# Performance work log

Hardware: AMD Instinct MI355X
Metric: run time of the kernel (lower is better)

Reference implementation:

```python
import jax, jax.numpy as jnp
import numpy as np

N, E = 50000, 800000          # nodes, edges (avg degree 16)
D_IN, D_H, D_OUT = 128, 128, 64
BN_EPS = 1e-5


def setup_inputs() -> dict:
    key = jax.random.key(0)
    ks = jax.random.split(key, 8)
    g = lambda k, shp, s: jax.random.normal(k, shp, jnp.float32) * s
    return {
        "x": jax.random.normal(ks[0], (N, D_IN), jnp.float32),
        "edge_index": jax.random.randint(ks[1], (2, E), 0, N),
        # SAGEConv layer 1: lin_l (neighbors, with bias), lin_r (root, no bias)
        "Wl1": g(ks[2], (D_IN, D_H), 0.05),
        "Wr1": g(ks[3], (D_IN, D_H), 0.05),
        "b1": jnp.zeros((D_H,), jnp.float32),
        # BatchNorm1d(hidden)
        "gamma": jnp.ones((D_H,), jnp.float32),
        "beta": jnp.zeros((D_H,), jnp.float32),
        # SAGEConv layer 2
        "Wl2": g(ks[4], (D_H, D_OUT), 0.05),
        "Wr2": g(ks[5], (D_H, D_OUT), 0.05),
        "b2": jnp.zeros((D_OUT,), jnp.float32),
    }


def _sage_conv(x, src, dst, Wl, Wr, b):
    """PyG SAGEConv (mean aggr): lin_l(mean_{j in N(i)} x_j) + lin_r(x_i)."""
    n = x.shape[0]
    agg = jax.ops.segment_sum(x[src], dst, num_segments=n)            # [N, d]
    cnt = jax.ops.segment_sum(jnp.ones((src.shape[0],), x.dtype), dst,
                              num_segments=n)                          # [N]
    agg = agg / jnp.maximum(cnt, 1.0)[:, None]                         # mean, 0 for isolated
    return agg @ Wl + x @ Wr + b


def _batch_norm(x, gamma, beta):
    """Training-mode BatchNorm1d: batch stats over the node axis, biased var."""
    mu = jnp.mean(x, axis=0)
    var = jnp.var(x, axis=0)
    return gamma * (x - mu) * jax.lax.rsqrt(var + BN_EPS) + beta


def reference(x, edge_index, Wl1, Wr1, b1, gamma, beta, Wl2, Wr2, b2):
    src, dst = edge_index[0], edge_index[1]
    h = _sage_conv(x, src, dst, Wl1, Wr1, b1)
    h = jax.nn.relu(_batch_norm(h, gamma, beta))
    # dropout is identity in eval / deterministic reference
    return _sage_conv(h, src, dst, Wl2, Wr2, b2)
```

## Files before the change

### kernel.cpp

```cpp
#include <hip/hip_runtime.h>
#include <hip/hip_bf16.h>
#include <hip/hip_fp8.h>

#define DIN   128
#define DH    128
#define DOUTC 64
#define BN_EPS 1e-5f

typedef __attribute__((ext_vector_type(8))) short bf16x8;
typedef __attribute__((ext_vector_type(4))) float f32x4;
typedef __attribute__((ext_vector_type(2))) float f32x2;

#ifndef __has_builtin
#define __has_builtin(x) 0
#endif
#if __has_builtin(__builtin_amdgcn_cvt_pk_f32_fp8) && __has_builtin(__builtin_amdgcn_cvt_pk_fp8_f32)
#define HW_FP8 1
#else
#define HW_FP8 0
#endif

__device__ inline unsigned short f2bf(float f) {
    __hip_bfloat16 b = __float2bfloat16(f);
    return *reinterpret_cast<unsigned short*>(&b);
}
__device__ inline float bf2f(unsigned short u) {
    return __uint_as_float(((unsigned int)u) << 16);
}
__device__ inline void fp8x4_to_f32(unsigned int w, float* o) {
#if HW_FP8
    f32x2 lo = __builtin_amdgcn_cvt_pk_f32_fp8((int)w, false);
    f32x2 hi = __builtin_amdgcn_cvt_pk_f32_fp8((int)w, true);
    o[0] = lo.x; o[1] = lo.y; o[2] = hi.x; o[3] = hi.y;
#else
    #pragma unroll
    for (int c = 0; c < 4; ++c) {
        __hip_fp8_e4m3 q; q.__x = (__hip_fp8_storage_t)((w >> (8 * c)) & 0xFF);
        o[c] = (float)q;
    }
#endif
}
__device__ inline unsigned int f32x4_to_fp8(float a, float b, float c, float d) {
#if HW_FP8
    int p = __builtin_amdgcn_cvt_pk_fp8_f32(a, b, 0, false);
    p = __builtin_amdgcn_cvt_pk_fp8_f32(c, d, p, true);
    return (unsigned int)p;
#else
    __hip_fp8_e4m3 qa(a), qb(b), qc(c), qd(d);
    return (unsigned int)qa.__x | ((unsigned int)qb.__x << 8) |
           ((unsigned int)qc.__x << 16) | ((unsigned int)qd.__x << 24);
#endif
}

__device__ inline void block_excl_scan_256(const int* __restrict__ arr,
                                           int* __restrict__ excl,
                                           int* __restrict__ wsum, int tid)
{
    int lane = tid & 63, w = tid >> 6;
    int v = arr[tid];
    int inc = v;
    #pragma unroll
    for (int off = 1; off < 64; off <<= 1) {
        int t = __shfl_up(inc, off, 64);
        if (lane >= off) inc += t;
    }
    if (lane == 63) wsum[w] = inc;
    __syncthreads();
    if (tid == 0) {
        int s = 0;
        #pragma unroll
        for (int i = 0; i < 4; ++i) { int t = wsum[i]; wsum[i] = s; s += t; }
    }
    __syncthreads();
    excl[tid] = inc - v + wsum[w];
    __syncthreads();
}

__global__ __launch_bounds__(256) void prep_kernel(
    const float* __restrict__ x, unsigned short* __restrict__ xb,
    unsigned char* __restrict__ xq,
    const float* __restrict__ Wl1, const float* __restrict__ Wr1,
    const float* __restrict__ Wl2, const float* __restrict__ Wr2,
    unsigned short* __restrict__ W1p, unsigned short* __restrict__ W2p,
    const int* __restrict__ ei, int* __restrict__ cursor,
    unsigned int* __restrict__ coarse,
    int total8, int cvtB, int E, int nb, int cap)
{
    __shared__ int hist[256], lstart[256], gbase[256], wsum[4];
    __shared__ unsigned int staged[4096];
    const int b = blockIdx.x;
    const int tid = threadIdx.x;

    if (b < cvtB) {
        int i = b * 256 + tid;
        if (i >= total8) return;
        float4 a = ((const float4*)x)[2 * i];
        float4 c = ((const float4*)x)[2 * i + 1];
        unsigned short t[8];
        t[0]=f2bf(a.x); t[1]=f2bf(a.y); t[2]=f2bf(a.z); t[3]=f2bf(a.w);
        t[4]=f2bf(c.x); t[5]=f2bf(c.y); t[6]=f2bf(c.z); t[7]=f2bf(c.w);
        *(uint4*)(xb + (size_t)i * 8) = *(uint4*)t;
        uint2 pk;
        pk.x = f32x4_to_fp8(a.x, a.y, a.z, a.w);
        pk.y = f32x4_to_fp8(c.x, c.y, c.z, c.w);
        *(uint2*)(xq + (size_t)i * 8) = pk;
        return;
    }
    if (b < cvtB + 192) {
        int region = (b - cvtB) >> 6;
        int idx = ((b - cvtB) & 63) * 256 + tid;
        int k = idx >> 7, c = idx & 127;
        int d = ((k >> 5) * 8 + (c >> 4)) * 512 + ((k >> 3) & 3) * 128 + (c & 15) * 8 + (k & 7);
        if (region == 0)      W1p[d] = f2bf(Wl1[idx]);
        else if (region == 1) W1p[128 * 128 + d] = f2bf(Wr1[idx]);
        else {
            float v = (c < 64) ? Wl2[k * 64 + c] : Wr2[k * 64 + (c - 64)];
            W2p[d] = f2bf(v);
        }
        return;
    }

    const int chunkBase = (b - cvtB - 192) * 4096;
    hist[tid] = 0;
    __syncthreads();

    unsigned int rec[16]; int pos[16]; int bb[16];
    #pragma unroll
    for (int i = 0; i < 16; ++i) {
        int e = chunkBase + i * 256 + tid;
        if (e < E) {
            int s = ei[e], d = ei[E + e];
            rec[i] = ((unsigned int)d << 16) | (unsigned int)s;
            bb[i]  = d >> 8;
            pos[i] = atomicAdd(&hist[bb[i]], 1);
        } else bb[i] = -1;
    }
    __syncthreads();

    block_excl_scan_256(hist, lstart, wsum, tid);

    if (tid < nb) {
        int c = hist[tid];
        gbase[tid] = c ? atomicAdd(&cursor[tid], c) : 0;
    }
    __syncthreads();

    #pragma unroll
    for (int i = 0; i < 16; ++i)
        if (bb[i] >= 0) staged[lstart[bb[i]] + pos[i]] = rec[i];
    __syncthreads();

    int total = min(4096, E - chunkBase);
    for (int i = tid; i < total; i += 256) {
        unsigned int r = staged[i];
        int bk  = (int)(r >> 24);
        int gp  = gbase[bk] + (i - lstart[bk]);
        if (gp < cap) coarse[(size_t)bk * cap + gp] = r;
    }
}

__global__ __launch_bounds__(256) void bin_fine(
    const int* __restrict__ cursor, const unsigned int* __restrict__ coarse,
    unsigned short* __restrict__ sorted, int* __restrict__ deg,
    int* __restrict__ row_start, int n, int cap)
{
    __shared__ int hist[256], pstart[256], cur2[256], wsum[4];
    const int b = blockIdx.x, tid = threadIdx.x;
    const int cnt = min(cursor[b], cap);
    const unsigned int* src = coarse + (size_t)b * cap;

    hist[tid] = 0;
    __syncthreads();

    int nIter = (cnt + 255) >> 8;
    for (int i = 0; i < nIter; ++i) {
        int idx = i * 256 + tid;
        if (idx < cnt) atomicAdd(&hist[(src[idx] >> 16) & 255], 1);
    }
    __syncthreads();

    block_excl_scan_256(hist, pstart, wsum, tid);
    cur2[tid] = pstart[tid];
    __syncthreads();

    for (int i = 0; i < nIter; ++i) {
        int idx = i * 256 + tid;
        if (idx < cnt) {
            unsigned int r = src[idx];
            int dl = (r >> 16) & 255;
            int p  = atomicAdd(&cur2[dl], 1);
            sorted[(size_t)b * cap + p] = (unsigned short)(r & 0xFFFFu);
        }
    }

    int node = b * 256 + tid;
    if (node < n) {
        deg[node]       = hist[tid];
        row_start[node] = b * cap + pstart[tid];
    }
}

__global__ __launch_bounds__(256) void gemm1_fused(
    const unsigned char* __restrict__ xq, const unsigned short* __restrict__ xb,
    const int* __restrict__ row_start, const int* __restrict__ deg,
    const unsigned short* __restrict__ sorted,
    const unsigned short* __restrict__ W1p, const float* __restrict__ bias,
    unsigned short* __restrict__ hb,
    float* __restrict__ bn_sum, float* __restrict__ bn_sumsq, int n)
{
    __shared__ unsigned short X[64][136];
    __shared__ unsigned short G[64][136];
    __shared__ float red[2][4][128];

    const int block_row = blockIdx.x * 64;
    const int tid  = threadIdx.x;
    const int wave = tid >> 6;
    const int lane = tid & 63;
    const int q    = lane >> 4;
    const int m16  = lane & 15;

    {
        int lr = wave * 16 + (lane >> 2);
        int g  = block_row + lr;
        #pragma unroll
        for (int i = 0; i < 4; ++i) {
            int c16 = (lane & 3) + 4 * i;
            uint4 v = {0u, 0u, 0u, 0u};
            if (g < n) v = ((const uint4*)(xb + (size_t)g * DIN))[c16];
            *(uint4*)&X[lr][c16 * 8] = v;
        }
    }

    {
        int sub = lane & 7, oct = lane >> 3;
        #pragma unroll
        for (int grp = 0; grp < 2; ++grp) {
            int lr = wave * 16 + grp * 8 + oct;
            int g  = block_row + lr;
            float acc[16];
            #pragma unroll
            for (int j = 0; j < 16; ++j) acc[j] = 0.f;
            int d = 0;
            if (g < n) {
                int base = row_start[g];
                d = deg[g];
                for (int t = 0; t < d; ++t) {
                    int s = (int)sorted[base + t];
                    uint4 raw = ((const uint4*)(xq + (size_t)s * DIN))[sub];
                    const unsigned int* w = (const unsigned int*)&raw;
                    #pragma unroll
                    for (int c = 0; c < 4; ++c) {
                        float o4[4];
                        fp8x4_to_f32(w[c], o4);
                        acc[c*4+0] += o4[0]; acc[c*4+1] += o4[1];
                        acc[c*4+2] += o4[2]; acc[c*4+3] += o4[3];
                    }
                }
            }
            float inv = 1.0f / fmaxf((float)d, 1.0f);
            unsigned short t16[16];
            #pragma unroll
            for (int j = 0; j < 16; ++j) t16[j] = f2bf(acc[j] * inv);
            *(uint4*)&G[lr][sub * 16]     = ((uint4*)t16)[0];
            *(uint4*)&G[lr][sub * 16 + 8] = ((uint4*)t16)[1];
        }
    }

    f32x4 acc[8];
    #pragma unroll
    for (int nt = 0; nt < 8; ++nt) acc[nt] = (f32x4){0.f, 0.f, 0.f, 0.f};

    #pragma unroll
    for (int ks = 0; ks < 4; ++ks) {
        bf16x8 ag = *(const bf16x8*)&G[wave * 16 + m16][ks * 32 + q * 8];
        const unsigned short* wp0 = W1p + (size_t)ks * 8 * 512;
        #pragma unroll
        for (int nt = 0; nt < 8; ++nt) {
            bf16x8 b = *(const bf16x8*)(wp0 + nt * 512 + lane * 8);
            acc[nt] = __builtin_amdgcn_mfma_f32_16x16x32_bf16(ag, b, acc[nt], 0, 0, 0);
        }
        bf16x8 ax = *(const bf16x8*)&X[wave * 16 + m16][ks * 32 + q * 8];
        const unsigned short* wp1 = W1p + (size_t)(4 + ks) * 8 * 512;
        #pragma unroll
        for (int nt = 0; nt < 8; ++nt) {
            bf16x8 b = *(const bf16x8*)(wp1 + nt * 512 + lane * 8);
            acc[nt] = __builtin_amdgcn_mfma_f32_16x16x32_bf16(ax, b, acc[nt], 0, 0, 0);
        }
    }

    float psum[8], psq[8];
    #pragma unroll
    for (int nt = 0; nt < 8; ++nt) {
        int col = nt * 16 + m16;
        float bv = bias[col];
        float s = 0.f, ssq = 0.f;
        #pragma unroll
        for (int reg = 0; reg < 4; ++reg) {
            int g = block_row + wave * 16 + q * 4 + reg;
            float v = acc[nt][reg] + bv;
            if (g < n) {
                hb[(size_t)g * DH + col] = f2bf(v);
                s += v; ssq += v * v;
            }
        }
        psum[nt] = s; psq[nt] = ssq;
    }
    #pragma unroll
    for (int nt = 0; nt < 8; ++nt) {
        psum[nt] += __shfl_xor(psum[nt], 16, 64);
        psum[nt] += __shfl_xor(psum[nt], 32, 64);
        psq[nt]  += __shfl_xor(psq[nt], 16, 64);
        psq[nt]  += __shfl_xor(psq[nt], 32, 64);
    }
    if (lane < 16) {
        #pragma unroll
        for (int nt = 0; nt < 8; ++nt) {
            red[0][wave][nt * 16 + lane] = psum[nt];
            red[1][wave][nt * 16 + lane] = psq[nt];
        }
    }
    __syncthreads();
    if (tid < 128) {
        float s = red[0][0][tid] + red[0][1][tid] + red[0][2][tid] + red[0][3][tid];
        float ssq = red[1][0][tid] + red[1][1][tid] + red[1][2][tid] + red[1][3][tid];
        atomicAdd(&bn_sum[tid], s);
        atomicAdd(&bn_sumsq[tid], ssq);
    }
}

__global__ __launch_bounds__(256) void gemm2p_mfma(
    const unsigned short* __restrict__ hb,
    const float* __restrict__ bn_sum, const float* __restrict__ bn_sumsq,
    const float* __restrict__ gamma, const float* __restrict__ beta,
    const unsigned short* __restrict__ W2p, const float* __restrict__ bias,
    unsigned short* __restrict__ P, float* __restrict__ out, int n)
{
    __shared__ unsigned short A[64][136];
    __shared__ float s_scale[128], s_shift[128];

    const int block_row = blockIdx.x * 64;
    const int tid  = threadIdx.x;
    const int wave = tid >> 6;
    const int lane = tid & 63;
    const int q    = lane >> 4;
    const int m16  = lane & 15;

    if (tid < 128) {
        float invN = 1.0f / (float)n;
        float mu  = bn_sum[tid] * invN;
        float var = bn_sumsq[tid] * invN - mu * mu;
        float sc  = gamma[tid] * rsqrtf(var + BN_EPS);
        s_scale[tid] = sc;
        s_shift[tid] = beta[tid] - mu * sc;
    }
    __syncthreads();

    {
        int lr = wave * 16 + (lane >> 2);
        int g  = block_row + lr;
        #pragma unroll
        for (int i = 0; i < 4; ++i) {
            int c16 = (lane & 3) + 4 * i;
            unsigned short t[8] = {0,0,0,0,0,0,0,0};
            if (g < n) {
                uint4 raw = ((const uint4*)(hb + (size_t)g * DH))[c16];
                const unsigned short* u = (const unsigned short*)&raw;
                #pragma unroll
                for (int j = 0; j < 8; ++j) {
                    int col = c16 * 8 + j;
                    float v = bf2f(u[j]) * s_scale[col] + s_shift[col];
                    t[j] = f2bf(fmaxf(v, 0.f));
                }
            }
            *(uint4*)&A[lr][c16 * 8] = *(uint4*)t;
        }
    }

    f32x4 acc[8];
    #pragma unroll
    for (int nt = 0; nt < 8; ++nt) acc[nt] = (f32x4){0.f, 0.f, 0.f, 0.f};

    #pragma unroll
    for (int ks = 0; ks < 4; ++ks) {
        bf16x8 a = *(const bf16x8*)&A[wave * 16 + m16][ks * 32 + q * 8];
        const unsigned short* wp = W2p + (size_t)ks * 8 * 512;
        #pragma unroll
        for (int nt = 0; nt < 8; ++nt) {
            bf16x8 b = *(const bf16x8*)(wp + nt * 512 + lane * 8);
            acc[nt] = __builtin_amdgcn_mfma_f32_16x16x32_bf16(a, b, acc[nt], 0, 0, 0);
        }
    }

    #pragma unroll
    for (int nt = 0; nt < 4; ++nt) {
        int col = nt * 16 + m16;
        #pragma unroll
        for (int reg = 0; reg < 4; ++reg) {
            int g = block_row + wave * 16 + q * 4 + reg;
            if (g < n) P[(size_t)g * DOUTC + col] = f2bf(acc[nt][reg]);
        }
    }
    #pragma unroll
    for (int nt = 4; nt < 8; ++nt) {
        int col = (nt - 4) * 16 + m16;
        float bv = bias[col];
        #pragma unroll
        for (int reg = 0; reg < 4; ++reg) {
            int g = block_row + wave * 16 + q * 4 + reg;
            if (g < n) out[(size_t)g * DOUTC + col] = acc[nt][reg] + bv;
        }
    }
}

__global__ __launch_bounds__(256) void agg_gather64_add(
    const int* __restrict__ row_start, const int* __restrict__ deg,
    const unsigned short* __restrict__ sorted, const unsigned short* __restrict__ P,
    float* __restrict__ out, int n)
{
    int wid  = (blockIdx.x * 256 + threadIdx.x) >> 6;
    int lane = threadIdx.x & 63;
    int sub = lane & 7, oct = lane >> 3;
    int r = wid * 8 + oct;
    if (r >= n) return;

    float acc[8];
    #pragma unroll
    for (int j = 0; j < 8; ++j) acc[j] = 0.f;

    int base = row_start[r];
    int d    = deg[r];
    for (int t = 0; t < d; ++t) {
        int s = (int)sorted[base + t];
        uint4 raw = ((const uint4*)(P + (size_t)s * DOUTC))[sub];
        const unsigned short* u = (const unsigned short*)&raw;
        #pragma unroll
        for (int j = 0; j < 8; ++j) acc[j] += bf2f(u[j]);
    }
    float inv = 1.0f / fmaxf((float)d, 1.0f);
    float* op = out + (size_t)r * DOUTC + sub * 8;
    float4 c0 = *(float4*)op;
    float4 c1 = *((float4*)op + 1);
    c0.x += acc[0] * inv; c0.y += acc[1] * inv;
    c0.z += acc[2] * inv; c0.w += acc[3] * inv;
    c1.x += acc[4] * inv; c1.y += acc[5] * inv;
    c1.z += acc[6] * inv; c1.w += acc[7] * inv;
    *(float4*)op = c0;
    *((float4*)op + 1) = c1;
}

extern "C" void kernel_launch(void* const* d_in, const int* in_sizes, int n_in,
                              void* d_out, int out_size, void* d_ws, size_t ws_size,
                              hipStream_t stream)
{
    const float* x     = (const float*)d_in[0];
    const int*   ei    = (const int*)  d_in[1];
    const float* Wl1   = (const float*)d_in[2];
    const float* Wr1   = (const float*)d_in[3];
    const float* b1    = (const float*)d_in[4];
    const float* gamma = (const float*)d_in[5];
    const float* beta  = (const float*)d_in[6];
    const float* Wl2   = (const float*)d_in[7];
    const float* Wr2   = (const float*)d_in[8];
    const float* b2    = (const float*)d_in[9];
    float*       out   = (float*)d_out;

    const int N = in_sizes[0] / DIN;
    const int E = in_sizes[1] / 2;

    const int NB  = (N + 255) >> 8;
    int cap = (E / NB) * 3 / 2 + 256;
    cap = (cap + 255) & ~255;

    float* bn_sum   = (float*)d_ws;
    float* bn_sumsq = bn_sum + DH;
    int* cursor     = (int*)(bn_sumsq + DH);
    int* deg        = cursor + 256;
    int* row_start  = deg + N;
    unsigned int* coarse   = (unsigned int*)(row_start + N);
    unsigned short* sorted = (unsigned short*)(coarse + (size_t)NB * cap);
    unsigned short* hb     = sorted + (size_t)NB * cap;
    unsigned short* xb     = hb + (size_t)N * DH;
    unsigned short* P      = xb + (size_t)N * DIN;
    unsigned short* W1p    = P + (size_t)N * DOUTC;
    unsigned short* W2p    = W1p + 256 * 128;
    unsigned char*  xq     = (unsigned char*)(W2p + 128 * 128);

    hipMemsetAsync(bn_sum, 0, (2 * DH + 256) * sizeof(float), stream);

    dim3 blk(256);
    const int cvtB        = (N * DIN / 8 + 255) / 256;
    const int binA_blocks = (E + 4095) / 4096;
    const int gemm_blocks = (N + 63) / 64;
    const int g64_blocks  = ((N + 7) / 8 + 3) / 4;

    prep_kernel<<<cvtB + 192 + binA_blocks, blk, 0, stream>>>(
        x, xb, xq, Wl1, Wr1, Wl2, Wr2, W1p, W2p,
        ei, cursor, coarse, N * DIN / 8, cvtB, E, NB, cap);

    bin_fine<<<NB, blk, 0, stream>>>(cursor, coarse, sorted, deg, row_start, N, cap);

    gemm1_fused<<<gemm_blocks, blk, 0, stream>>>(xq, xb, row_start, deg, sorted,
                                                 W1p, b1, hb, bn_sum, bn_sumsq, N);

    gemm2p_mfma<<<gemm_blocks, blk, 0, stream>>>(hb, bn_sum, bn_sumsq,
                                                 gamma, beta, W2p, b2, P, out, N);

    agg_gather64_add<<<g64_blocks, blk, 0, stream>>>(row_start, deg, sorted,
                                                     P, out, N);
}
```

Before: 214.3 us.

## Drop bf16 copy of x, load operands directly into MFMA regs, batch gathers

The prep kernel no longer writes a bf16 copy of x. gemm1 instead reads the fp32 x rows straight from global memory into MFMA A-operand registers and converts them there. gemm2 likewise applies BN+ReLU directly in registers instead of staging through LDS. The neighbor-gather loops in gemm1 and the final aggregation are unrolled by 8 so that several independent row loads are in flight at once. This cuts one N×128 bf16 write and read plus the LDS staging, at the cost of reading fp32 x, which is twice the bytes per row, with less coalesced per-lane access, and higher register pressure.

```diff
diff --git a/kernel.cpp b/kernel.cpp
--- a/kernel.cpp
+++ b/kernel.cpp
@@ -77,8 +77,7 @@
 }
 
 __global__ __launch_bounds__(256) void prep_kernel(
-    const float* __restrict__ x, unsigned short* __restrict__ xb,
-    unsigned char* __restrict__ xq,
+    const float* __restrict__ x, unsigned char* __restrict__ xq,
     const float* __restrict__ Wl1, const float* __restrict__ Wr1,
     const float* __restrict__ Wl2, const float* __restrict__ Wr2,
     unsigned short* __restrict__ W1p, unsigned short* __restrict__ W2p,
@@ -96,10 +95,6 @@
         if (i >= total8) return;
         float4 a = ((const float4*)x)[2 * i];
         float4 c = ((const float4*)x)[2 * i + 1];
-        unsigned short t[8];
-        t[0]=f2bf(a.x); t[1]=f2bf(a.y); t[2]=f2bf(a.z); t[3]=f2bf(a.w);
-        t[4]=f2bf(c.x); t[5]=f2bf(c.y); t[6]=f2bf(c.z); t[7]=f2bf(c.w);
-        *(uint4*)(xb + (size_t)i * 8) = *(uint4*)t;
         uint2 pk;
         pk.x = f32x4_to_fp8(a.x, a.y, a.z, a.w);
         pk.y = f32x4_to_fp8(c.x, c.y, c.z, c.w);
@@ -201,14 +196,13 @@
 }
 
 __global__ __launch_bounds__(256) void gemm1_fused(
-    const unsigned char* __restrict__ xq, const unsigned short* __restrict__ xb,
+    const unsigned char* __restrict__ xq, const float* __restrict__ x,
     const int* __restrict__ row_start, const int* __restrict__ deg,
     const unsigned short* __restrict__ sorted,
     const unsigned short* __restrict__ W1p, const float* __restrict__ bias,
     unsigned short* __restrict__ hb,
     float* __restrict__ bn_sum, float* __restrict__ bn_sumsq, int n)
 {
-    __shared__ unsigned short X[64][136];
     __shared__ unsigned short G[64][136];
     __shared__ float red[2][4][128];
 
@@ -218,18 +212,6 @@
     const int lane = tid & 63;
     const int q    = lane >> 4;
     const int m16  = lane & 15;
-
-    {
-        int lr = wave * 16 + (lane >> 2);
-        int g  = block_row + lr;
-        #pragma unroll
-        for (int i = 0; i < 4; ++i) {
-            int c16 = (lane & 3) + 4 * i;
-            uint4 v = {0u, 0u, 0u, 0u};
-            if (g < n) v = ((const uint4*)(xb + (size_t)g * DIN))[c16];
-            *(uint4*)&X[lr][c16 * 8] = v;
-        }
-    }
 
     {
         int sub = lane & 7, oct = lane >> 3;
@@ -244,7 +226,27 @@
             if (g < n) {
                 int base = row_start[g];
                 d = deg[g];
-                for (int t = 0; t < d; ++t) {
+                int t = 0;
+                for (; t + 8 <= d; t += 8) {
+                    uint4 raws[8];
+                    #pragma unroll
+                    for (int u = 0; u < 8; ++u) {
+                        int s = (int)sorted[base + t + u];
+                        raws[u] = ((const uint4*)(xq + (size_t)s * DIN))[sub];
+                    }
+                    #pragma unroll
+                    for (int u = 0; u < 8; ++u) {
+                        const unsigned int* w = (const unsigned int*)&raws[u];
+                        #pragma unroll
+                        for (int c = 0; c < 4; ++c) {
+                            float o4[4];
+                            fp8x4_to_f32(w[c], o4);
+                            acc[c*4+0] += o4[0]; acc[c*4+1] += o4[1];
+                            acc[c*4+2] += o4[2]; acc[c*4+3] += o4[3];
+                        }
+                    }
+                }
+                for (; t < d; ++t) {
                     int s = (int)sorted[base + t];
                     uint4 raw = ((const uint4*)(xq + (size_t)s * DIN))[sub];
                     const unsigned int* w = (const unsigned int*)&raw;
@@ -270,6 +272,7 @@
     #pragma unroll
     for (int nt = 0; nt < 8; ++nt) acc[nt] = (f32x4){0.f, 0.f, 0.f, 0.f};
 
+    const int grow = block_row + wave * 16 + m16;
     #pragma unroll
     for (int ks = 0; ks < 4; ++ks) {
         bf16x8 ag = *(const bf16x8*)&G[wave * 16 + m16][ks * 32 + q * 8];
@@ -279,7 +282,19 @@
             bf16x8 b = *(const bf16x8*)(wp0 + nt * 512 + lane * 8);
             acc[nt] = __builtin_amdgcn_mfma_f32_16x16x32_bf16(ag, b, acc[nt], 0, 0, 0);
         }
-        bf16x8 ax = *(const bf16x8*)&X[wave * 16 + m16][ks * 32 + q * 8];
+        bf16x8 ax;
+        {
+            float4 f0 = {0.f,0.f,0.f,0.f}, f1 = {0.f,0.f,0.f,0.f};
+            if (grow < n) {
+                const float* xr = x + (size_t)grow * DIN + ks * 32 + q * 8;
+                f0 = *(const float4*)xr;
+                f1 = *(const float4*)(xr + 4);
+            }
+            unsigned short t[8];
+            t[0]=f2bf(f0.x); t[1]=f2bf(f0.y); t[2]=f2bf(f0.z); t[3]=f2bf(f0.w);
+            t[4]=f2bf(f1.x); t[5]=f2bf(f1.y); t[6]=f2bf(f1.z); t[7]=f2bf(f1.w);
+            ax = *(bf16x8*)t;
+        }
         const unsigned short* wp1 = W1p + (size_t)(4 + ks) * 8 * 512;
         #pragma unroll
         for (int nt = 0; nt < 8; ++nt) {
@@ -335,7 +350,6 @@
     const unsigned short* __restrict__ W2p, const float* __restrict__ bias,
     unsigned short* __restrict__ P, float* __restrict__ out, int n)
 {
-    __shared__ unsigned short A[64][136];
     __shared__ float s_scale[128], s_shift[128];
 
     const int block_row = blockIdx.x * 64;
@@ -355,34 +369,35 @@
     }
     __syncthreads();
 
-    {
-        int lr = wave * 16 + (lane >> 2);
-        int g  = block_row + lr;
-        #pragma unroll
-        for (int i = 0; i < 4; ++i) {
-            int c16 = (lane & 3) + 4 * i;
+    f32x4 acc[8];
+    #pragma unroll
+    for (int nt = 0; nt < 8; ++nt) acc[nt] = (f32x4){0.f, 0.f, 0.f, 0.f};
+
+    const int grow = block_row + wave * 16 + m16;
+    #pragma unroll
+    for (int ks = 0; ks < 4; ++ks) {
+        bf16x8 a;
+        {
+            int kbase = ks * 32 + q * 8;
+            float4 sc0 = *(const float4*)&s_scale[kbase];
+            float4 sc1 = *(const float4*)&s_scale[kbase + 4];
+            float4 sh0 = *(const float4*)&s_shift[kbase];
+            float4 sh1 = *(const float4*)&s_shift[kbase + 4];
             unsigned short t[8] = {0,0,0,0,0,0,0,0};
-            if (g < n) {
-                uint4 raw = ((const uint4*)(hb + (size_t)g * DH))[c16];
+            if (grow < n) {
+                uint4 raw = *(const uint4*)(hb + (size_t)grow * DH + kbase);
                 const unsigned short* u = (const unsigned short*)&raw;
-                #pragma unroll
-                for (int j = 0; j < 8; ++j) {
-                    int col = c16 * 8 + j;
-                    float v = bf2f(u[j]) * s_scale[col] + s_shift[col];
-                    t[j] = f2bf(fmaxf(v, 0.f));
-                }
+                t[0] = f2bf(fmaxf(bf2f(u[0]) * sc0.x + sh0.x, 0.f));
+                t[1] = f2bf(fmaxf(bf2f(u[1]) * sc0.y + sh0.y, 0.f));
+                t[2] = f2bf(fmaxf(bf2f(u[2]) * sc0.z + sh0.z, 0.f));
+                t[3] = f2bf(fmaxf(bf2f(u[3]) * sc0.w + sh0.w, 0.f));
+                t[4] = f2bf(fmaxf(bf2f(u[4]) * sc1.x + sh1.x, 0.f));
+                t[5] = f2bf(fmaxf(bf2f(u[5]) * sc1.y + sh1.y, 0.f));
+                t[6] = f2bf(fmaxf(bf2f(u[6]) * sc1.z + sh1.z, 0.f));
+                t[7] = f2bf(fmaxf(bf2f(u[7]) * sc1.w + sh1.w, 0.f));
             }
-            *(uint4*)&A[lr][c16 * 8] = *(uint4*)t;
-        }
-    }
-
-    f32x4 acc[8];
-    #pragma unroll
-    for (int nt = 0; nt < 8; ++nt) acc[nt] = (f32x4){0.f, 0.f, 0.f, 0.f};
-
-    #pragma unroll
-    for (int ks = 0; ks < 4; ++ks) {
-        bf16x8 a = *(const bf16x8*)&A[wave * 16 + m16][ks * 32 + q * 8];
+            a = *(bf16x8*)t;
+        }
         const unsigned short* wp = W2p + (size_t)ks * 8 * 512;
         #pragma unroll
         for (int nt = 0; nt < 8; ++nt) {
@@ -429,12 +444,27 @@
 
     int base = row_start[r];
     int d    = deg[r];
-    for (int t = 0; t < d; ++t) {
+    int t = 0;
+    for (; t + 8 <= d; t += 8) {
+        uint4 raws[8];
+        #pragma unroll
+        for (int u = 0; u < 8; ++u) {
+            int s = (int)sorted[base + t + u];
+            raws[u] = ((const uint4*)(P + (size_t)s * DOUTC))[sub];
+        }
+        #pragma unroll
+        for (int u = 0; u < 8; ++u) {
+            const unsigned short* us = (const unsigned short*)&raws[u];
+            #pragma unroll
+            for (int j = 0; j < 8; ++j) acc[j] += bf2f(us[j]);
+        }
+    }
+    for (; t < d; ++t) {
         int s = (int)sorted[base + t];
         uint4 raw = ((const uint4*)(P + (size_t)s * DOUTC))[sub];
-        const unsigned short* u = (const unsigned short*)&raw;
-        #pragma unroll
-        for (int j = 0; j < 8; ++j) acc[j] += bf2f(u[j]);
+        const unsigned short* us = (const unsigned short*)&raw;
+        #pragma unroll
+        for (int j = 0; j < 8; ++j) acc[j] += bf2f(us[j]);
     }
     float inv = 1.0f / fmaxf((float)d, 1.0f);
     float* op = out + (size_t)r * DOUTC + sub * 8;
@@ -479,8 +509,7 @@
     unsigned int* coarse   = (unsigned int*)(row_start + N);
     unsigned short* sorted = (unsigned short*)(coarse + (size_t)NB * cap);
     unsigned short* hb     = sorted + (size_t)NB * cap;
-    unsigned short* xb     = hb + (size_t)N * DH;
-    unsigned short* P      = xb + (size_t)N * DIN;
+    unsigned short* P      = hb + (size_t)N * DH;
     unsigned short* W1p    = P + (size_t)N * DOUTC;
     unsigned short* W2p    = W1p + 256 * 128;
     unsigned char*  xq     = (unsigned char*)(W2p + 128 * 128);
@@ -494,12 +523,12 @@
     const int g64_blocks  = ((N + 7) / 8 + 3) / 4;
 
     prep_kernel<<<cvtB + 192 + binA_blocks, blk, 0, stream>>>(
-        x, xb, xq, Wl1, Wr1, Wl2, Wr2, W1p, W2p,
+        x, xq, Wl1, Wr1, Wl2, Wr2, W1p, W2p,
         ei, cursor, coarse, N * DIN / 8, cvtB, E, NB, cap);
 
     bin_fine<<<NB, blk, 0, stream>>>(cursor, coarse, sorted, deg, row_start, N, cap);
 
-    gemm1_fused<<<gemm_blocks, blk, 0, stream>>>(xq, xb, row_start, deg, sorted,
+    gemm1_fused<<<gemm_blocks, blk, 0, stream>>>(xq, x, row_start, deg, sorted,
                                                  W1p, b1, hb, bn_sum, bn_sumsq, N);
 
     gemm2p_mfma<<<gemm_blocks, blk, 0, stream>>>(hb, bn_sum, bn_sumsq,
```

Measured after the change: 209.1 us. -2.4%, faster.
